# Kernel tuning notes

Measured on AMD Instinct MI355X. Metric: run time of the kernel, lower is better.

The kernel has to match this reference:

```python
import jax, jax.numpy as jnp
import numpy as np

B, L, N, E, LAT = 128, 336, 321, 128, 64


def setup_inputs() -> dict:
    key = jax.random.key(0)
    ks = jax.random.split(key, 8)
    s_e = 1.0 / np.sqrt(L)
    s_l = 1.0 / np.sqrt(E)
    return {
        "x": jax.random.normal(ks[0], (B, L, N), dtype=jnp.float32),
        "time_x": jax.random.normal(ks[1], (B, N, E), dtype=jnp.float32),
        "W_embed": jax.random.uniform(ks[2], (N, L, E), jnp.float32, -s_e, s_e),
        "b_embed": jax.random.uniform(ks[3], (N, E), jnp.float32, -s_e, s_e),
        "W_mu": jax.random.uniform(ks[4], (N, E, LAT), jnp.float32, -s_l, s_l),
        "b_mu": jax.random.uniform(ks[5], (N, LAT), jnp.float32, -s_l, s_l),
        "W_var": jax.random.uniform(ks[6], (N, E, LAT), jnp.float32, -s_l, s_l),
        "b_var": jax.random.uniform(ks[7], (N, LAT), jnp.float32, -s_l, s_l),
    }


def reference(x, time_x, W_embed, b_embed, W_mu, b_mu, W_var, b_var):
    # x: [B, L, N] -> per-channel layout [B, N, L]
    xp = jnp.transpose(x, (0, 2, 1))
    # grouped GEMM over channels: h[b,n,e] = sum_l xp[b,n,l] * W_embed[n,l,e]
    h = jnp.einsum("bnl,nle->bne", xp, W_embed) + b_embed[None, :, :]
    h_hat = jax.nn.sigmoid(time_x) * h
    mu_h_hat = jnp.einsum("bne,nek->bnk", h_hat, W_mu) + b_mu[None, :, :]
    var_h_hat = jnp.einsum("bne,nek->bnk", h_hat, W_var) + b_var[None, :, :]
    return (h, h_hat, mu_h_hat, var_h_hat)
```

## Files before the change

### kernel.cpp

```cpp
#include <hip/hip_runtime.h>
#include <math.h>

#define B_   128
#define L_   336
#define N_   321
#define E_   128
#define LAT_ 64

typedef float f4 __attribute__((ext_vector_type(4)));

#define OUT_HH  (B_*N_*E_)
#define OUT_MU  (2*B_*N_*E_)
#define OUT_VAR (2*B_*N_*E_ + B_*N_*LAT_)

__global__ __launch_bounds__(256) void k_transpose(const float* __restrict__ x,
                                                   float* __restrict__ xp2) {
    __shared__ float t[4][32][33];
    const int n0 = blockIdx.x * 32;
    const int b0 = blockIdx.y * 32;
    const int l0 = blockIdx.z * 4;
    const int tid = threadIdx.x;
    const int tn = tid & 31;
    const int tb = tid >> 5;
    const int nn = n0 + tn;

    if (nn < N_) {
#pragma unroll
        for (int l = 0; l < 4; ++l)
#pragma unroll
            for (int p = 0; p < 4; ++p) {
                const int b = b0 + tb + 8 * p;
                t[l][tn][tb + 8 * p] = x[(size_t)b * (L_ * N_) + (size_t)(l0 + l) * N_ + nn];
            }
    }
    __syncthreads();
#pragma unroll
    for (int p = 0; p < 4; ++p) {
        const int idx = tid + 256 * p;
        const int row = idx >> 3;
        const int bq  = idx & 7;
        const int l   = row >> 5;
        const int n2  = row & 31;
        if (n0 + n2 < N_) {
            f4 v;
#pragma unroll
            for (int j = 0; j < 4; ++j) v[j] = t[l][n2][bq * 4 + j];
            *(f4*)(xp2 + (size_t)(n0 + n2) * (L_ * B_) + (size_t)(l0 + l) * B_ + b0 + bq * 4) = v;
        }
    }
}

#define KT 16

template <bool XP>
__global__ __launch_bounds__(256, 3) void k_fused(const float* __restrict__ xsrc,
                                                  const float* __restrict__ time_x,
                                                  const float* __restrict__ W_embed,
                                                  const float* __restrict__ b_embed,
                                                  const float* __restrict__ W_mu,
                                                  const float* __restrict__ b_mu,
                                                  const float* __restrict__ W_var,
                                                  const float* __restrict__ b_var,
                                                  float* __restrict__ out) {
    __shared__ float A2t[128 * 64];
    __shared__ float Wbuf[KT * 128];
    float* A1 = A2t;

    const int tid  = threadIdx.x;
    const int tx   = tid & 31;
    const int trow = tid >> 5;

    int bid = blockIdx.x;
    {
        const int nwg = N_ * 2, q = nwg / 8, r = nwg % 8;
        const int xcd = bid % 8, lid = bid / 8;
        bid = (xcd < r ? xcd * (q + 1) : r * (q + 1) + (xcd - r) * q) + lid;
    }
    const int n  = bid >> 1;
    const int b0 = (bid & 1) * 64;

    float acc[8][4];
#pragma unroll
    for (int i = 0; i < 8; ++i)
#pragma unroll
        for (int j = 0; j < 4; ++j) acc[i][j] = 0.f;

    const int akk = tid >> 4, arq = tid & 15;
    const int wk0 = tid >> 5, wc0 = tid & 31;

    for (int k0 = 0; k0 < L_; k0 += KT) {
        f4 av;
        if (XP) {
            av = *(const f4*)(xsrc + (size_t)n * (L_ * B_) + (size_t)(k0 + akk) * B_ + b0 + arq * 4);
        } else {
#pragma unroll
            for (int j = 0; j < 4; ++j) {
                const int r = arq * 4 + j;
                av[j] = xsrc[(size_t)(b0 + r) * (L_ * N_) + (size_t)(k0 + akk) * N_ + n];
            }
        }
        f4 wv0 = *(const f4*)(W_embed + (size_t)n * (L_ * E_) + (size_t)(k0 + wk0) * E_ + wc0 * 4);
        f4 wv1 = *(const f4*)(W_embed + (size_t)n * (L_ * E_) + (size_t)(k0 + wk0 + 8) * E_ + wc0 * 4);

        __syncthreads();
        *(f4*)(A1 + akk * 64 + arq * 4) = av;
        *(f4*)(Wbuf + wk0 * 128 + wc0 * 4) = wv0;
        *(f4*)(Wbuf + (wk0 + 8) * 128 + wc0 * 4) = wv1;
        __syncthreads();

#pragma unroll
        for (int kk = 0; kk < KT; ++kk) {
            f4 a0 = *(const f4*)(A1 + kk * 64 + trow * 8);
            f4 a1 = *(const f4*)(A1 + kk * 64 + trow * 8 + 4);
            f4 w  = *(const f4*)(Wbuf + kk * 128 + tx * 4);
#pragma unroll
            for (int i = 0; i < 4; ++i)
#pragma unroll
                for (int j = 0; j < 4; ++j) {
                    acc[i][j]     += a0[i] * w[j];
                    acc[i + 4][j] += a1[i] * w[j];
                }
        }
    }
    __syncthreads();

    f4 bev = *(const f4*)(b_embed + n * E_ + tx * 4);
    f4 hh[8];
#pragma unroll
    for (int i = 0; i < 8; ++i) {
        const int row = b0 + trow * 8 + i;
        const size_t base = ((size_t)row * N_ + n) * E_ + tx * 4;
        f4 h;
#pragma unroll
        for (int j = 0; j < 4; ++j) h[j] = acc[i][j] + bev[j];
        *(f4*)(out + base) = h;
        f4 tv = *(const f4*)(time_x + base);
        f4 hv;
#pragma unroll
        for (int j = 0; j < 4; ++j) hv[j] = h[j] * (1.f / (1.f + expf(-tv[j])));
        *(f4*)(out + OUT_HH + base) = hv;
        hh[i] = hv;
    }
#pragma unroll
    for (int c = 0; c < 2; ++c) {
#pragma unroll
        for (int j = 0; j < 4; ++j) {
            const int e  = tx * 4 + j;
            const int pc = (2 * trow + c) ^ (e & 15);
            f4 v;
#pragma unroll
            for (int q = 0; q < 4; ++q) v[q] = hh[4 * c + q][j];
            *(f4*)(A2t + e * 64 + pc * 4) = v;
        }
    }

#pragma unroll
    for (int i = 0; i < 8; ++i)
#pragma unroll
        for (int j = 0; j < 4; ++j) acc[i][j] = 0.f;

    for (int e0 = 0; e0 < E_; e0 += KT) {
        f4 wv[2];
#pragma unroll
        for (int t = 0; t < 2; ++t) {
            const int kk  = wk0 + 8 * t;
            const int col = wc0 * 4;
            const float* src = (col < 64)
                ? (W_mu  + (size_t)n * (E_ * LAT_) + (size_t)(e0 + kk) * LAT_ + col)
                : (W_var + (size_t)n * (E_ * LAT_) + (size_t)(e0 + kk) * LAT_ + (col - 64));
            wv[t] = *(const f4*)src;
        }
        __syncthreads();
        *(f4*)(Wbuf + wk0 * 128 + wc0 * 4) = wv[0];
        *(f4*)(Wbuf + (wk0 + 8) * 128 + wc0 * 4) = wv[1];
        __syncthreads();

#pragma unroll
        for (int kk = 0; kk < KT; ++kk) {
            const int e = e0 + kk;
            f4 a0 = *(const f4*)(A2t + e * 64 + ((2 * trow + 0) ^ (e & 15)) * 4);
            f4 a1 = *(const f4*)(A2t + e * 64 + ((2 * trow + 1) ^ (e & 15)) * 4);
            f4 w  = *(const f4*)(Wbuf + kk * 128 + tx * 4);
#pragma unroll
            for (int i = 0; i < 4; ++i)
#pragma unroll
                for (int j = 0; j < 4; ++j) {
                    acc[i][j]     += a0[i] * w[j];
                    acc[i + 4][j] += a1[i] * w[j];
                }
        }
    }

    f4 bb;
    if (tx < 16) bb = *(const f4*)(b_mu  + n * LAT_ + tx * 4);
    else         bb = *(const f4*)(b_var + n * LAT_ + (tx - 16) * 4);
#pragma unroll
    for (int i = 0; i < 8; ++i) {
        const int row = b0 + trow * 8 + i;
        const size_t base = ((size_t)row * N_ + n) * LAT_;
        f4 o;
#pragma unroll
        for (int j = 0; j < 4; ++j) o[j] = acc[i][j] + bb[j];
        if (tx < 16) *(f4*)(out + OUT_MU  + base + tx * 4) = o;
        else         *(f4*)(out + OUT_VAR + base + (tx - 16) * 4) = o;
    }
}

extern "C" void kernel_launch(void* const* d_in, const int* in_sizes, int n_in,
                              void* d_out, int out_size, void* d_ws, size_t ws_size,
                              hipStream_t stream) {
    const float* x       = (const float*)d_in[0];
    const float* time_x  = (const float*)d_in[1];
    const float* W_embed = (const float*)d_in[2];
    const float* b_embed = (const float*)d_in[3];
    const float* W_mu    = (const float*)d_in[4];
    const float* b_mu    = (const float*)d_in[5];
    const float* W_var   = (const float*)d_in[6];
    const float* b_var   = (const float*)d_in[7];
    float* out = (float*)d_out;

    const size_t need = (size_t)N_ * L_ * B_ * sizeof(float);
    const int nblk = N_ * 2;

    if (ws_size >= need) {
        float* xp2 = (float*)d_ws;
        k_transpose<<<dim3(11, 4, 84), 256, 0, stream>>>(x, xp2);
        k_fused<true><<<nblk, 256, 0, stream>>>(xp2, time_x, W_embed, b_embed,
                                                W_mu, b_mu, W_var, b_var, out);
    } else {
        k_fused<false><<<nblk, 256, 0, stream>>>(x, time_x, W_embed, b_embed,
                                                 W_mu, b_mu, W_var, b_var, out);
    }
}
```

Before: 254.0 us.

## Halve batch tile per block, widen K tile, register-prefetch next chunk

Each block now covers 32 batch rows instead of 64, so the grid grows to four blocks per channel. The K tile grows to 32, and the next chunk of x and weights is prefetched into registers while the current chunk is computed, in both GEMM phases. Occupancy is raised through launch bounds and the smaller accumulator. Output stores become nontemporal and expf becomes __expf. The trade-off is that the per-channel weights are reread by four blocks instead of two, and each block does less arithmetic per shared-memory load.

```diff
diff --git a/kernel.cpp b/kernel.cpp
--- a/kernel.cpp
+++ b/kernel.cpp
@@ -50,10 +50,11 @@
     }
 }
 
-#define KT 16
+#define KT  32
+#define NCH ((L_ + KT - 1) / KT)
 
 template <bool XP>
-__global__ __launch_bounds__(256, 3) void k_fused(const float* __restrict__ xsrc,
+__global__ __launch_bounds__(256, 5) void k_fused(const float* __restrict__ xsrc,
                                                   const float* __restrict__ time_x,
                                                   const float* __restrict__ W_embed,
                                                   const float* __restrict__ b_embed,
@@ -62,7 +63,7 @@
                                                   const float* __restrict__ W_var,
                                                   const float* __restrict__ b_var,
                                                   float* __restrict__ out) {
-    __shared__ float A2t[128 * 64];
+    __shared__ float A2t[128 * 32];
     __shared__ float Wbuf[KT * 128];
     float* A1 = A2t;
 
@@ -72,137 +73,169 @@
 
     int bid = blockIdx.x;
     {
-        const int nwg = N_ * 2, q = nwg / 8, r = nwg % 8;
-        const int xcd = bid % 8, lid = bid / 8;
+        const int nwg = N_ * 4, q = nwg / 8, r = nwg % 8;
+        const int xcd = bid & 7, lid = bid >> 3;
         bid = (xcd < r ? xcd * (q + 1) : r * (q + 1) + (xcd - r) * q) + lid;
     }
-    const int n  = bid >> 1;
-    const int b0 = (bid & 1) * 64;
-
-    float acc[8][4];
-#pragma unroll
-    for (int i = 0; i < 8; ++i)
+    const int n  = bid >> 2;
+    const int b0 = (bid & 3) * 32;
+
+    const int al = tid >> 3;
+    const int ab = tid & 7;
+    const int wr = tid >> 5;
+    const int wc = tid & 31;
+
+    const float* Wemb  = W_embed + (size_t)n * (L_ * E_);
+    const float* Wmu_n = W_mu  + (size_t)n * (E_ * LAT_);
+    const float* Wvar_n= W_var + (size_t)n * (E_ * LAT_);
+
+    float acc[4][4];
+#pragma unroll
+    for (int i = 0; i < 4; ++i)
 #pragma unroll
         for (int j = 0; j < 4; ++j) acc[i][j] = 0.f;
 
-    const int akk = tid >> 4, arq = tid & 15;
-    const int wk0 = tid >> 5, wc0 = tid & 31;
-
-    for (int k0 = 0; k0 < L_; k0 += KT) {
-        f4 av;
+    f4 rA, rW[4];
+    {
+        const int k = al;
         if (XP) {
-            av = *(const f4*)(xsrc + (size_t)n * (L_ * B_) + (size_t)(k0 + akk) * B_ + b0 + arq * 4);
+            rA = *(const f4*)(xsrc + (size_t)n * (L_ * B_) + (size_t)k * B_ + b0 + ab * 4);
         } else {
 #pragma unroll
-            for (int j = 0; j < 4; ++j) {
-                const int r = arq * 4 + j;
-                av[j] = xsrc[(size_t)(b0 + r) * (L_ * N_) + (size_t)(k0 + akk) * N_ + n];
-            }
-        }
-        f4 wv0 = *(const f4*)(W_embed + (size_t)n * (L_ * E_) + (size_t)(k0 + wk0) * E_ + wc0 * 4);
-        f4 wv1 = *(const f4*)(W_embed + (size_t)n * (L_ * E_) + (size_t)(k0 + wk0 + 8) * E_ + wc0 * 4);
-
-        __syncthreads();
-        *(f4*)(A1 + akk * 64 + arq * 4) = av;
-        *(f4*)(Wbuf + wk0 * 128 + wc0 * 4) = wv0;
-        *(f4*)(Wbuf + (wk0 + 8) * 128 + wc0 * 4) = wv1;
-        __syncthreads();
+            for (int j = 0; j < 4; ++j)
+                rA[j] = xsrc[(size_t)(b0 + ab * 4 + j) * (L_ * N_) + (size_t)k * N_ + n];
+        }
+#pragma unroll
+        for (int p = 0; p < 4; ++p)
+            rW[p] = *(const f4*)(Wemb + (size_t)(wr + 8 * p) * E_ + wc * 4);
+    }
+
+    for (int it = 0; it < NCH; ++it) {
+        __syncthreads();
+        *(f4*)(A1 + al * 32 + ab * 4) = rA;
+#pragma unroll
+        for (int p = 0; p < 4; ++p)
+            *(f4*)(Wbuf + (wr + 8 * p) * 128 + wc * 4) = rW[p];
+        __syncthreads();
+
+        if (it + 1 < NCH) {
+            const int k0 = (it + 1) * KT;
+            const int k  = k0 + al;
+            f4 z = {0.f, 0.f, 0.f, 0.f};
+            if (k < L_) {
+                if (XP) {
+                    z = *(const f4*)(xsrc + (size_t)n * (L_ * B_) + (size_t)k * B_ + b0 + ab * 4);
+                } else {
+#pragma unroll
+                    for (int j = 0; j < 4; ++j)
+                        z[j] = xsrc[(size_t)(b0 + ab * 4 + j) * (L_ * N_) + (size_t)k * N_ + n];
+                }
+            }
+            rA = z;
+#pragma unroll
+            for (int p = 0; p < 4; ++p) {
+                const int kw = k0 + wr + 8 * p;
+                f4 zw = {0.f, 0.f, 0.f, 0.f};
+                if (kw < L_) zw = *(const f4*)(Wemb + (size_t)kw * E_ + wc * 4);
+                rW[p] = zw;
+            }
+        }
 
 #pragma unroll
         for (int kk = 0; kk < KT; ++kk) {
-            f4 a0 = *(const f4*)(A1 + kk * 64 + trow * 8);
-            f4 a1 = *(const f4*)(A1 + kk * 64 + trow * 8 + 4);
-            f4 w  = *(const f4*)(Wbuf + kk * 128 + tx * 4);
+            f4 a = *(const f4*)(A1 + kk * 32 + trow * 4);
+            f4 w = *(const f4*)(Wbuf + kk * 128 + tx * 4);
 #pragma unroll
             for (int i = 0; i < 4; ++i)
 #pragma unroll
-                for (int j = 0; j < 4; ++j) {
-                    acc[i][j]     += a0[i] * w[j];
-                    acc[i + 4][j] += a1[i] * w[j];
-                }
+                for (int j = 0; j < 4; ++j) acc[i][j] += a[i] * w[j];
         }
     }
     __syncthreads();
 
+    {
+#pragma unroll
+        for (int p = 0; p < 4; ++p) {
+            const int e = wr + 8 * p;
+            rW[p] = (wc < 16) ? *(const f4*)(Wmu_n  + (size_t)e * LAT_ + wc * 4)
+                              : *(const f4*)(Wvar_n + (size_t)e * LAT_ + wc * 4 - 64);
+        }
+    }
+
     f4 bev = *(const f4*)(b_embed + n * E_ + tx * 4);
-    f4 hh[8];
-#pragma unroll
-    for (int i = 0; i < 8; ++i) {
-        const int row = b0 + trow * 8 + i;
+    f4 hh[4];
+#pragma unroll
+    for (int i = 0; i < 4; ++i) {
+        const int row = b0 + trow * 4 + i;
         const size_t base = ((size_t)row * N_ + n) * E_ + tx * 4;
         f4 h;
 #pragma unroll
         for (int j = 0; j < 4; ++j) h[j] = acc[i][j] + bev[j];
-        *(f4*)(out + base) = h;
+        __builtin_nontemporal_store(h, (f4*)(out + base));
         f4 tv = *(const f4*)(time_x + base);
         f4 hv;
 #pragma unroll
-        for (int j = 0; j < 4; ++j) hv[j] = h[j] * (1.f / (1.f + expf(-tv[j])));
-        *(f4*)(out + OUT_HH + base) = hv;
+        for (int j = 0; j < 4; ++j) hv[j] = h[j] * (1.f / (1.f + __expf(-tv[j])));
+        __builtin_nontemporal_store(hv, (f4*)(out + OUT_HH + base));
         hh[i] = hv;
     }
-#pragma unroll
-    for (int c = 0; c < 2; ++c) {
+    {
+        const int slotw = trow ^ (tx & 7);
 #pragma unroll
         for (int j = 0; j < 4; ++j) {
-            const int e  = tx * 4 + j;
-            const int pc = (2 * trow + c) ^ (e & 15);
+            const int e = tx * 4 + j;
             f4 v;
 #pragma unroll
-            for (int q = 0; q < 4; ++q) v[q] = hh[4 * c + q][j];
-            *(f4*)(A2t + e * 64 + pc * 4) = v;
-        }
-    }
-
-#pragma unroll
-    for (int i = 0; i < 8; ++i)
+            for (int q = 0; q < 4; ++q) v[q] = hh[q][j];
+            *(f4*)(A2t + e * 32 + slotw * 4) = v;
+        }
+    }
+
+#pragma unroll
+    for (int i = 0; i < 4; ++i)
 #pragma unroll
         for (int j = 0; j < 4; ++j) acc[i][j] = 0.f;
 
-    for (int e0 = 0; e0 < E_; e0 += KT) {
-        f4 wv[2];
-#pragma unroll
-        for (int t = 0; t < 2; ++t) {
-            const int kk  = wk0 + 8 * t;
-            const int col = wc0 * 4;
-            const float* src = (col < 64)
-                ? (W_mu  + (size_t)n * (E_ * LAT_) + (size_t)(e0 + kk) * LAT_ + col)
-                : (W_var + (size_t)n * (E_ * LAT_) + (size_t)(e0 + kk) * LAT_ + (col - 64));
-            wv[t] = *(const f4*)src;
-        }
-        __syncthreads();
-        *(f4*)(Wbuf + wk0 * 128 + wc0 * 4) = wv[0];
-        *(f4*)(Wbuf + (wk0 + 8) * 128 + wc0 * 4) = wv[1];
-        __syncthreads();
+    for (int c = 0; c < 4; ++c) {
+        __syncthreads();
+#pragma unroll
+        for (int p = 0; p < 4; ++p)
+            *(f4*)(Wbuf + (wr + 8 * p) * 128 + wc * 4) = rW[p];
+        __syncthreads();
+
+        if (c + 1 < 4) {
+            const int e0 = (c + 1) * KT;
+#pragma unroll
+            for (int p = 0; p < 4; ++p) {
+                const int e = e0 + wr + 8 * p;
+                rW[p] = (wc < 16) ? *(const f4*)(Wmu_n  + (size_t)e * LAT_ + wc * 4)
+                                  : *(const f4*)(Wvar_n + (size_t)e * LAT_ + wc * 4 - 64);
+            }
+        }
 
 #pragma unroll
         for (int kk = 0; kk < KT; ++kk) {
-            const int e = e0 + kk;
-            f4 a0 = *(const f4*)(A2t + e * 64 + ((2 * trow + 0) ^ (e & 15)) * 4);
-            f4 a1 = *(const f4*)(A2t + e * 64 + ((2 * trow + 1) ^ (e & 15)) * 4);
-            f4 w  = *(const f4*)(Wbuf + kk * 128 + tx * 4);
+            const int slot = trow ^ (kk >> 2);
+            f4 a = *(const f4*)(A2t + (c * KT + kk) * 32 + slot * 4);
+            f4 w = *(const f4*)(Wbuf + kk * 128 + tx * 4);
 #pragma unroll
             for (int i = 0; i < 4; ++i)
 #pragma unroll
-                for (int j = 0; j < 4; ++j) {
-                    acc[i][j]     += a0[i] * w[j];
-                    acc[i + 4][j] += a1[i] * w[j];
-                }
-        }
-    }
-
-    f4 bb;
-    if (tx < 16) bb = *(const f4*)(b_mu  + n * LAT_ + tx * 4);
-    else         bb = *(const f4*)(b_var + n * LAT_ + (tx - 16) * 4);
-#pragma unroll
-    for (int i = 0; i < 8; ++i) {
-        const int row = b0 + trow * 8 + i;
+                for (int j = 0; j < 4; ++j) acc[i][j] += a[i] * w[j];
+        }
+    }
+
+    f4 bb = (tx < 16) ? *(const f4*)(b_mu  + n * LAT_ + tx * 4)
+                      : *(const f4*)(b_var + n * LAT_ + tx * 4 - 64);
+#pragma unroll
+    for (int i = 0; i < 4; ++i) {
+        const int row = b0 + trow * 4 + i;
         const size_t base = ((size_t)row * N_ + n) * LAT_;
         f4 o;
 #pragma unroll
         for (int j = 0; j < 4; ++j) o[j] = acc[i][j] + bb[j];
-        if (tx < 16) *(f4*)(out + OUT_MU  + base + tx * 4) = o;
-        else         *(f4*)(out + OUT_VAR + base + (tx - 16) * 4) = o;
+        if (tx < 16) __builtin_nontemporal_store(o, (f4*)(out + OUT_MU  + base + tx * 4));
+        else         __builtin_nontemporal_store(o, (f4*)(out + OUT_VAR + base + tx * 4 - 64));
     }
 }
 
@@ -220,7 +253,7 @@
     float* out = (float*)d_out;
 
     const size_t need = (size_t)N_ * L_ * B_ * sizeof(float);
-    const int nblk = N_ * 2;
+    const int nblk = N_ * 4;
 
     if (ws_size >= need) {
         float* xp2 = (float*)d_ws;
```

Measured after the change: 704.2 us. 2.77x slower.
